# Kernel optimization log

Measured on AMD Instinct MI355X. Metric: run time of the kernel, lower is better.

Reference implementation:

```python
import jax, jax.numpy as jnp
import numpy as np

N_HEAD = 16
ROPE_BASE = 10000.0


def apply_rope(x):
    # x: [B, T, H, D], torchtune interleaved-pair RoPE
    B, T, H, D = x.shape
    pos = jnp.arange(T, dtype=jnp.float32)
    freqs = 1.0 / (ROPE_BASE ** (jnp.arange(0, D, 2, dtype=jnp.float32) / D))  # [D/2]
    theta = pos[:, None] * freqs[None, :]            # [T, D/2]
    cos = jnp.cos(theta)[None, :, None, :]           # [1, T, 1, D/2]
    sin = jnp.sin(theta)[None, :, None, :]
    xp = x.reshape(B, T, H, D // 2, 2)
    x0, x1 = xp[..., 0], xp[..., 1]
    out = jnp.stack([x0 * cos - x1 * sin, x1 * cos + x0 * sin], axis=-1)
    return out.reshape(B, T, H, D).astype(x.dtype)


def setup_inputs() -> dict:
    key = jax.random.key(0)
    k1, k2, k3 = jax.random.split(key, 3)
    B, T, C = 4, 2048, 1024
    x = jax.random.normal(k1, (B, T, C), dtype=jnp.float32)
    w_qkv = jax.random.normal(k2, (C, 3 * C), dtype=jnp.float32) * 0.02
    b_qkv = jnp.zeros((3 * C,), dtype=jnp.float32)
    w_proj = jax.random.normal(k3, (C, C), dtype=jnp.float32) * 0.02
    b_proj = jnp.zeros((C,), dtype=jnp.float32)
    return {"x": x, "w_qkv": w_qkv, "b_qkv": b_qkv, "w_proj": w_proj, "b_proj": b_proj}


def reference(x, w_qkv, b_qkv, w_proj, b_proj):
    B, T, C = x.shape
    H = N_HEAD
    D = C // H
    qkv = x @ w_qkv + b_qkv                          # [B, T, 3C]
    q, k, v = jnp.split(qkv, 3, axis=-1)
    q = apply_rope(q.reshape(B, T, H, D))
    k = apply_rope(k.reshape(B, T, H, D))
    v = v.reshape(B, T, H, D)
    scale = 1.0 / jnp.sqrt(jnp.asarray(D, dtype=x.dtype))
    attn = jnp.einsum('bthd,bshd->bhts', q, k) * scale  # [B, H, T, T] (non-causal)
    attn = jax.nn.softmax(attn, axis=-1)
    out = jnp.einsum('bhts,bshd->bthd', attn, v).reshape(B, T, C)
    return out @ w_proj + b_proj
```

## Files before the change

### kernel.cpp

```cpp
#include <hip/hip_runtime.h>

typedef unsigned short ushort_t;
typedef unsigned int   uint_t;
typedef __attribute__((ext_vector_type(8))) short bf16x8;
typedef __attribute__((ext_vector_type(4))) float f32x4;

__device__ __forceinline__ ushort_t f2bf(float f) {
    union { float f; uint_t i; } x; x.f = f;
    uint_t i = x.i + 0x7fffu + ((x.i >> 16) & 1u);
    return (ushort_t)(i >> 16);
}
__device__ __forceinline__ ushort_t f2bf_trunc(float f) {
    union { float f; uint_t i; } x; x.f = f;
    return (ushort_t)(x.i >> 16);
}
__device__ __forceinline__ void async16(const void* g, void* l) {
    __builtin_amdgcn_global_load_lds(
        (const __attribute__((address_space(1))) uint_t*)g,
        (__attribute__((address_space(3))) uint_t*)l, 16, 0, 0);
}

__global__ __launch_bounds__(256) void conv_bf16(
    const float* __restrict__ in, ushort_t* __restrict__ outp)
{
    int i = (blockIdx.x * 256 + threadIdx.x) * 4;
    float4 v = *(const float4*)(in + i);
    uint_t a = (uint_t)f2bf(v.x) | ((uint_t)f2bf(v.y) << 16);
    uint_t b = (uint_t)f2bf(v.z) | ((uint_t)f2bf(v.w) << 16);
    uint2 st = { a, b };
    *(uint2*)(outp + i) = st;
}

__global__ __launch_bounds__(256) void transpose_conv(
    const float* __restrict__ in, ushort_t* __restrict__ outp, int R, int C)
{
    __shared__ ushort_t t[64][65];
    int r0 = blockIdx.y * 64, c0 = blockIdx.x * 64;
    int lr = threadIdx.x >> 4, lc = (threadIdx.x & 15) * 4;
#pragma unroll
    for (int rr = 0; rr < 4; ++rr) {
        float4 v = *(const float4*)(in + (size_t)(r0 + rr * 16 + lr) * C + c0 + lc);
        t[lc + 0][rr * 16 + lr] = f2bf(v.x);
        t[lc + 1][rr * 16 + lr] = f2bf(v.y);
        t[lc + 2][rr * 16 + lr] = f2bf(v.z);
        t[lc + 3][rr * 16 + lr] = f2bf(v.w);
    }
    __syncthreads();
    int oc = threadIdx.x >> 2, och = (threadIdx.x & 3) * 16;
    union { uint4 v[2]; ushort_t u[16]; } pk;
#pragma unroll
    for (int j = 0; j < 16; ++j) pk.u[j] = t[oc][och + j];
    uint4* dst = (uint4*)(outp + (size_t)(c0 + oc) * R + r0 + och);
    dst[0] = pk.v[0]; dst[1] = pk.v[1];
}

__global__ __launch_bounds__(256) void rope_table_k(float2* __restrict__ tab)
{
    int idx = blockIdx.x * 256 + threadIdx.x;
    int t = idx >> 5, i = idx & 31;
    float freq = powf(10000.0f, -(float)i * (1.0f / 32.0f));
    float sn, cs;
    sincosf((float)t * freq, &sn, &cs);
    tab[idx] = make_float2(cs, sn);
}

template <int MODE>
__global__ __launch_bounds__(256) void gemm_mfma(
    const ushort_t* __restrict__ A, const ushort_t* __restrict__ Bt,
    const float* __restrict__ bias, void* __restrict__ Cv,
    const float2* __restrict__ tab, int M, int N, int K, int coloff)
{
    __shared__ ushort_t As[128][64];
    __shared__ ushort_t Bs[128][64];
    const int tid = threadIdx.x;
    const int w = tid >> 6, lane = tid & 63, ln = lane & 15, quad = lane >> 4;
    const int wm = w >> 1, wn = w & 1;
    const int row0 = blockIdx.y * 128, col0 = blockIdx.x * 128 + coloff;

    f32x4 acc[4][4] = {};

    const int swch = (lane & 7) ^ (lane >> 3);
    const ushort_t* ga = A  + (size_t)(row0 + w * 8 + (lane >> 3)) * K + swch * 8;
    const ushort_t* gb = Bt + (size_t)(col0 + w * 8 + (lane >> 3)) * K + swch * 8;
    ushort_t* la = &As[w * 8][0];
    ushort_t* lb = &Bs[w * 8][0];
    const int rch0 = ln & 7;

    for (int k0 = 0; k0 < K; k0 += 64) {
#pragma unroll
        for (int j = 0; j < 4; ++j) {
            async16(ga + (size_t)(j * 32) * K + k0, la + j * 32 * 64);
            async16(gb + (size_t)(j * 32) * K + k0, lb + j * 32 * 64);
        }
        __syncthreads();
#pragma unroll
        for (int kk = 0; kk < 2; ++kk) {
            int ch = ((kk * 4 + quad) ^ rch0) * 8;
            bf16x8 af[4], bfv[4];
#pragma unroll
            for (int mt = 0; mt < 4; ++mt)
                af[mt] = *(const bf16x8*)&As[wm * 64 + mt * 16 + ln][ch];
#pragma unroll
            for (int nt = 0; nt < 4; ++nt)
                bfv[nt] = *(const bf16x8*)&Bs[wn * 64 + nt * 16 + ln][ch];
#pragma unroll
            for (int mt = 0; mt < 4; ++mt)
#pragma unroll
                for (int nt = 0; nt < 4; ++nt) {
                    if (MODE == 2)
                        acc[mt][nt] = __builtin_amdgcn_mfma_f32_16x16x32_bf16(
                            af[mt], bfv[nt], acc[mt][nt], 0, 0, 0);
                    else
                        acc[mt][nt] = __builtin_amdgcn_mfma_f32_16x16x32_bf16(
                            bfv[nt], af[mt], acc[mt][nt], 0, 0, 0);
                }
        }
        __syncthreads();
    }

    if (MODE == 2) {
#pragma unroll
        for (int nt = 0; nt < 4; ++nt) {
            int c = col0 + wn * 64 + nt * 16 + ln;
            float bv = bias[c];
            int c2 = c - 2048;
            size_t vrow = ((size_t)(c2 >> 6)) * 64 + (c2 & 63);
#pragma unroll
            for (int mt = 0; mt < 4; ++mt) {
                int rr = row0 + wm * 64 + mt * 16 + quad * 4;
                int b = rr >> 11, t0 = rr & 2047;
                uint2 st;
                st.x = (uint_t)f2bf(acc[mt][nt][0] + bv)
                     | ((uint_t)f2bf(acc[mt][nt][1] + bv) << 16);
                st.y = (uint_t)f2bf(acc[mt][nt][2] + bv)
                     | ((uint_t)f2bf(acc[mt][nt][3] + bv) << 16);
                *(uint2*)((ushort_t*)Cv + ((size_t)b * 16 * 64 + vrow) * 2048 + t0) = st;
            }
        }
    } else {
#pragma unroll
        for (int mt = 0; mt < 4; ++mt) {
            int rr = row0 + wm * 64 + mt * 16 + ln;
#pragma unroll
            for (int nt = 0; nt < 4; ++nt) {
                int c0 = col0 + wn * 64 + nt * 16 + quad * 4;
                float4 bv = *(const float4*)(bias + c0);
                float v0 = acc[mt][nt][0] + bv.x, v1 = acc[mt][nt][1] + bv.y;
                float v2 = acc[mt][nt][2] + bv.z, v3 = acc[mt][nt][3] + bv.w;
                if (MODE == 1) {
                    int i0 = (c0 & 63) >> 1;
                    const float2* trow = tab + (size_t)(rr & 2047) * 32;
                    float2 cs0 = trow[i0], cs1 = trow[i0 + 1];
                    float o0 = v0 * cs0.x - v1 * cs0.y;
                    float o1 = v1 * cs0.x + v0 * cs0.y;
                    float o2 = v2 * cs1.x - v3 * cs1.y;
                    float o3 = v3 * cs1.x + v2 * cs1.y;
                    uint2 st;
                    st.x = (uint_t)f2bf(o0) | ((uint_t)f2bf(o1) << 16);
                    st.y = (uint_t)f2bf(o2) | ((uint_t)f2bf(o3) << 16);
                    *(uint2*)((ushort_t*)Cv + (size_t)rr * N + c0) = st;
                } else {
                    float4 st = { v0, v1, v2, v3 };
                    *(float4*)((float*)Cv + (size_t)rr * N + c0) = st;
                }
            }
        }
    }
}

__global__ __launch_bounds__(512, 4) void attn_mfma(
    const ushort_t* __restrict__ qkv, const ushort_t* __restrict__ vtg,
    ushort_t* __restrict__ outp)
{
    __shared__ ushort_t Ks[2][64][64];
    __shared__ ushort_t Vts[2][64][64];
    __shared__ ushort_t Ps[8][16][72];

    const int tid = threadIdx.x;
    const int w = tid >> 6, lane = tid & 63, ln = lane & 15, quad = lane >> 4;
    const int bh = blockIdx.x, qt = blockIdx.y, b = bh >> 4, h = bh & 15;
    const size_t base = (size_t)b * 2048 * 3072 + h * 64;

    bf16x8 af[2][2];
#pragma unroll
    for (int s = 0; s < 2; ++s)
#pragma unroll
        for (int kk = 0; kk < 2; ++kk)
            af[s][kk] = *(const bf16x8*)(qkv + base
                + (size_t)(qt * 256 + w * 32 + s * 16 + ln) * 3072 + kk * 32 + quad * 8);

    bf16x8 ones;
#pragma unroll
    for (int j = 0; j < 8; ++j) ones[j] = (short)0x3F80;

    f32x4 oaccT[2][4] = {};
    f32x4 oneacc[2] = {};
    const float SC = 0.125f * 1.44269504f;

    const int swch = (lane & 7) ^ (lane >> 3);
    const ushort_t* kg = qkv + base + 1024 + (size_t)(lane >> 3) * 3072 + swch * 8;
    const ushort_t* vg = vtg + ((size_t)bh * 64 + (lane >> 3)) * 2048 + swch * 8;
    const int rch0 = ln & 7;
    const int r8 = w * 8;

    async16(kg, &Ks[0][r8][0]);
    async16(vg + (size_t)r8 * 2048, &Vts[0][r8][0]);
    async16(kg + (size_t)r8 * 3072, &Ks[0][r8][0]);
    asm volatile("s_waitcnt vmcnt(0)" ::: "memory");
    __builtin_amdgcn_s_barrier();

    int cur = 0;
    for (int kt = 0; kt < 32; ++kt) {
        if (kt < 31) {
            async16(kg + (size_t)((kt + 1) * 64 + r8) * 3072, &Ks[cur ^ 1][r8][0]);
            async16(vg + (size_t)r8 * 2048 + (kt + 1) * 64, &Vts[cur ^ 1][r8][0]);
        }

        bf16x8 vf[2][4];
#pragma unroll
        for (int kk = 0; kk < 2; ++kk) {
            int ch = ((kk * 4 + quad) ^ rch0) * 8;
#pragma unroll
            for (int nt = 0; nt < 4; ++nt)
                vf[kk][nt] = *(const bf16x8*)&Vts[cur][nt * 16 + ln][ch];
        }

#pragma unroll
        for (int s = 0; s < 2; ++s) {
            f32x4 sacc[4] = {};
#pragma unroll
            for (int kk = 0; kk < 2; ++kk) {
                int ch = ((kk * 4 + quad) ^ rch0) * 8;
#pragma unroll
                for (int nt = 0; nt < 4; ++nt) {
                    bf16x8 bfv = *(const bf16x8*)&Ks[cur][nt * 16 + ln][ch];
                    sacc[nt] = __builtin_amdgcn_mfma_f32_16x16x32_bf16(
                        af[s][kk], bfv, sacc[nt], 0, 0, 0);
                }
            }

            if (s == 1)
                asm volatile("s_waitcnt lgkmcnt(0)" ::: "memory");
#pragma unroll
            for (int nt = 0; nt < 4; ++nt)
#pragma unroll
                for (int r = 0; r < 4; ++r)
                    Ps[w][quad * 4 + r][nt * 16 + ln] =
                        f2bf_trunc(exp2f(fmaf(sacc[nt][r], SC, -24.0f)));
            asm volatile("s_waitcnt lgkmcnt(0)" ::: "memory");

#pragma unroll
            for (int kk = 0; kk < 2; ++kk) {
                bf16x8 pf = *(const bf16x8*)&Ps[w][ln][kk * 32 + quad * 8];
                oneacc[s] = __builtin_amdgcn_mfma_f32_16x16x32_bf16(
                    ones, pf, oneacc[s], 0, 0, 0);
#pragma unroll
                for (int nt = 0; nt < 4; ++nt)
                    oaccT[s][nt] = __builtin_amdgcn_mfma_f32_16x16x32_bf16(
                        vf[kk][nt], pf, oaccT[s][nt], 0, 0, 0);
            }
        }

        asm volatile("s_waitcnt vmcnt(0) lgkmcnt(0)" ::: "memory");
        __builtin_amdgcn_s_barrier();
        cur ^= 1;
    }

#pragma unroll
    for (int s = 0; s < 2; ++s) {
        float linv = 1.0f / oneacc[s][0];
        size_t row = (size_t)b * 2048 + qt * 256 + w * 32 + s * 16 + ln;
#pragma unroll
        for (int nt = 0; nt < 4; ++nt) {
            uint2 st;
            st.x = (uint_t)f2bf(oaccT[s][nt][0] * linv)
                 | ((uint_t)f2bf(oaccT[s][nt][1] * linv) << 16);
            st.y = (uint_t)f2bf(oaccT[s][nt][2] * linv)
                 | ((uint_t)f2bf(oaccT[s][nt][3] * linv) << 16);
            *(uint2*)(outp + row * 1024 + h * 64 + nt * 16 + quad * 4) = st;
        }
    }
}

extern "C" void kernel_launch(void* const* d_in, const int* in_sizes, int n_in,
                              void* d_out, int out_size, void* d_ws, size_t ws_size,
                              hipStream_t stream)
{
    (void)in_sizes; (void)n_in; (void)out_size; (void)ws_size;

    const float* x      = (const float*)d_in[0];
    const float* w_qkv  = (const float*)d_in[1];
    const float* b_qkv  = (const float*)d_in[2];
    const float* w_proj = (const float*)d_in[3];
    const float* b_proj = (const float*)d_in[4];
    float*       out    = (float*)d_out;

    ushort_t* x_bf    = (ushort_t*)d_ws;
    ushort_t* wqkvT   = x_bf    + (size_t)8192 * 1024;
    ushort_t* wprojT  = wqkvT   + (size_t)3072 * 1024;
    ushort_t* qkv_bf  = wprojT  + (size_t)1024 * 1024;
    ushort_t* attn_bf = qkv_bf  + (size_t)8192 * 3072;
    ushort_t* vtg     = attn_bf + (size_t)8192 * 1024;
    float2*   tab     = (float2*)(vtg + (size_t)64 * 64 * 2048);

    conv_bf16<<<8192, 256, 0, stream>>>(x, x_bf);
    transpose_conv<<<dim3(48, 16), 256, 0, stream>>>(w_qkv, wqkvT, 1024, 3072);
    transpose_conv<<<dim3(16, 16), 256, 0, stream>>>(w_proj, wprojT, 1024, 1024);
    rope_table_k<<<256, 256, 0, stream>>>(tab);

    gemm_mfma<1><<<dim3(16, 64), 256, 0, stream>>>(
        x_bf, wqkvT, b_qkv, qkv_bf, tab, 8192, 3072, 1024, 0);

    gemm_mfma<2><<<dim3(8, 64), 256, 0, stream>>>(
        x_bf, wqkvT, b_qkv, vtg, nullptr, 8192, 3072, 1024, 2048);

    attn_mfma<<<dim3(64, 8), 512, 0, stream>>>(qkv_bf, vtg, attn_bf);

    gemm_mfma<0><<<dim3(8, 64), 256, 0, stream>>>(
        attn_bf, wprojT, b_proj, out, nullptr, 8192, 1024, 1024, 0);
}
```

Baseline: 326.5 us.

## Transpose score MFMA to enable packed bf16 P stores and hoist K fragment loads

```diff
diff --git a/kernel.cpp b/kernel.cpp
--- a/kernel.cpp
+++ b/kernel.cpp
@@ -10,9 +10,10 @@
     uint_t i = x.i + 0x7fffu + ((x.i >> 16) & 1u);
     return (ushort_t)(i >> 16);
 }
-__device__ __forceinline__ ushort_t f2bf_trunc(float f) {
-    union { float f; uint_t i; } x; x.f = f;
-    return (ushort_t)(x.i >> 16);
+__device__ __forceinline__ uint_t cvt_pk_bf16(float lo, float hi) {
+    uint_t r;
+    asm("v_cvt_pk_bf16_f32 %0, %1, %2" : "=v"(r) : "v"(lo), "v"(hi));
+    return r;
 }
 __device__ __forceinline__ void async16(const void* g, void* l) {
     __builtin_amdgcn_global_load_lds(
@@ -203,9 +204,8 @@
     const int rch0 = ln & 7;
     const int r8 = w * 8;
 
-    async16(kg, &Ks[0][r8][0]);
+    async16(kg + (size_t)r8 * 3072, &Ks[0][r8][0]);
     async16(vg + (size_t)r8 * 2048, &Vts[0][r8][0]);
-    async16(kg + (size_t)r8 * 3072, &Ks[0][r8][0]);
     asm volatile("s_waitcnt vmcnt(0)" ::: "memory");
     __builtin_amdgcn_s_barrier();
 
@@ -216,37 +216,40 @@
             async16(vg + (size_t)r8 * 2048 + (kt + 1) * 64, &Vts[cur ^ 1][r8][0]);
         }
 
-        bf16x8 vf[2][4];
+        bf16x8 kf[2][4], vf[2][4];
 #pragma unroll
         for (int kk = 0; kk < 2; ++kk) {
             int ch = ((kk * 4 + quad) ^ rch0) * 8;
 #pragma unroll
-            for (int nt = 0; nt < 4; ++nt)
+            for (int nt = 0; nt < 4; ++nt) {
+                kf[kk][nt] = *(const bf16x8*)&Ks[cur][nt * 16 + ln][ch];
                 vf[kk][nt] = *(const bf16x8*)&Vts[cur][nt * 16 + ln][ch];
+            }
         }
 
 #pragma unroll
         for (int s = 0; s < 2; ++s) {
             f32x4 sacc[4] = {};
 #pragma unroll
-            for (int kk = 0; kk < 2; ++kk) {
-                int ch = ((kk * 4 + quad) ^ rch0) * 8;
-#pragma unroll
-                for (int nt = 0; nt < 4; ++nt) {
-                    bf16x8 bfv = *(const bf16x8*)&Ks[cur][nt * 16 + ln][ch];
+            for (int kk = 0; kk < 2; ++kk)
+#pragma unroll
+                for (int nt = 0; nt < 4; ++nt)
                     sacc[nt] = __builtin_amdgcn_mfma_f32_16x16x32_bf16(
-                        af[s][kk], bfv, sacc[nt], 0, 0, 0);
-                }
-            }
+                        kf[kk][nt], af[s][kk], sacc[nt], 0, 0, 0);
 
             if (s == 1)
                 asm volatile("s_waitcnt lgkmcnt(0)" ::: "memory");
 #pragma unroll
-            for (int nt = 0; nt < 4; ++nt)
-#pragma unroll
-                for (int r = 0; r < 4; ++r)
-                    Ps[w][quad * 4 + r][nt * 16 + ln] =
-                        f2bf_trunc(exp2f(fmaf(sacc[nt][r], SC, -24.0f)));
+            for (int nt = 0; nt < 4; ++nt) {
+                float e0 = exp2f(fmaf(sacc[nt][0], SC, -24.0f));
+                float e1 = exp2f(fmaf(sacc[nt][1], SC, -24.0f));
+                float e2 = exp2f(fmaf(sacc[nt][2], SC, -24.0f));
+                float e3 = exp2f(fmaf(sacc[nt][3], SC, -24.0f));
+                uint2 pk;
+                pk.x = cvt_pk_bf16(e0, e1);
+                pk.y = cvt_pk_bf16(e2, e3);
+                *(uint2*)&Ps[w][ln][nt * 16 + quad * 4] = pk;
+            }
             asm volatile("s_waitcnt lgkmcnt(0)" ::: "memory");
 
 #pragma unroll
```

Measured after the change: 320.7 us. Within noise of the previous version (-1.8%).
